# Optimization experiments

Measured on AMD Instinct MI355X. Metric: run time of the kernel, lower is better.

## Reference

```python
import jax, jax.numpy as jnp
import numpy as np

START = 1
NUM_CLASSES = 64  # labels drawn from [0, 64)
EPS = 1e-12       # matches F.normalize eps


def _compactness_loss(embeddings, labels):
    # L2-normalize each embedding (F.normalize, dim=-1)
    norms = jnp.maximum(jnp.linalg.norm(embeddings, axis=-1, keepdims=True), EPS)
    emb = embeddings / norms  # [N, D]

    ones = jnp.ones((emb.shape[0],), dtype=emb.dtype)
    counts = jax.ops.segment_sum(ones, labels, num_segments=NUM_CLASSES)      # [C]
    sums = jax.ops.segment_sum(emb, labels, num_segments=NUM_CLASSES)         # [C, D]

    # per-class mean, then L2-normalize the center (F.normalize, dim=1)
    centers = sums / jnp.maximum(counts, 1.0)[:, None]
    c_norms = jnp.maximum(jnp.linalg.norm(centers, axis=-1, keepdims=True), EPS)
    centers = centers / c_norms  # [C, D]

    # cosine similarity of each sample to its own class center
    sim = jnp.sum(emb * centers[labels], axis=-1)  # [N]

    # per-class mean of (1 - sim), only classes with count > 1 contribute
    per_class_sum = jax.ops.segment_sum(1.0 - sim, labels, num_segments=NUM_CLASSES)  # [C]
    valid = counts > 1.0
    class_loss = jnp.where(valid, per_class_sum / jnp.maximum(counts, 1.0), 0.0)
    n_valid = jnp.sum(valid.astype(emb.dtype))
    return jnp.where(n_valid > 0, jnp.sum(class_loss) / jnp.maximum(n_valid, 1.0), 0.0)


def setup_inputs() -> dict:
    key = jax.random.key(0)
    k1, k2 = jax.random.split(key)
    N, D = 262144, 256
    embeddings = jax.random.normal(k1, (N, D), dtype=jnp.float32)
    labels = jax.random.randint(k2, (N,), 0, NUM_CLASSES, dtype=jnp.int64)
    return {"embeddings": embeddings, "labels": labels, "epoch": 5}


def reference(embeddings, labels, epoch):
    if epoch < START:  # epoch is a static python int
        return jnp.asarray(0.0, dtype=embeddings.dtype)
    return _compactness_loss(embeddings, labels)
```

## Files before the change

### kernel.cpp

```cpp
#include <hip/hip_runtime.h>

#define CLS   64
#define DIM   256
#define PARTS 8
#define HB    256
#define HT    256

typedef float f32x4 __attribute__((ext_vector_type(4)));

__device__ __forceinline__ float wave_sum64(float f) {
    int t;
    t = __builtin_amdgcn_update_dpp(0, __float_as_int(f), 0x111, 0xf, 0xf, false); f += __int_as_float(t);
    t = __builtin_amdgcn_update_dpp(0, __float_as_int(f), 0x112, 0xf, 0xf, false); f += __int_as_float(t);
    t = __builtin_amdgcn_update_dpp(0, __float_as_int(f), 0x114, 0xf, 0xe, false); f += __int_as_float(t);
    t = __builtin_amdgcn_update_dpp(0, __float_as_int(f), 0x118, 0xf, 0xc, false); f += __int_as_float(t);
    t = __builtin_amdgcn_update_dpp(0, __float_as_int(f), 0x142, 0xa, 0xf, false); f += __int_as_float(t);
    t = __builtin_amdgcn_update_dpp(0, __float_as_int(f), 0x143, 0xc, 0xf, false); f += __int_as_float(t);
    return __int_as_float(__builtin_amdgcn_readlane(__float_as_int(f), 63));
}

__global__ __launch_bounds__(HT) void k_hist(const int* __restrict__ labels, int N,
                                             int* __restrict__ hist)
{
    __shared__ int h[CLS];
    if (threadIdx.x < CLS) h[threadIdx.x] = 0;
    __syncthreads();
    const int chunk = (N + gridDim.x - 1) / gridDim.x;
    const int s = blockIdx.x * chunk;
    const int e = min(N, s + chunk);
    for (int i = s + threadIdx.x; i < e; i += blockDim.x)
        atomicAdd(&h[labels[i]], 1);
    __syncthreads();
    if (threadIdx.x < CLS) hist[blockIdx.x * CLS + threadIdx.x] = h[threadIdx.x];
}

__global__ __launch_bounds__(HT) void k_scatter2(
    const int* __restrict__ labels, int N,
    const int* __restrict__ hist,
    int* __restrict__ cstart,
    int* __restrict__ bucket)
{
    __shared__ int t4[4][CLS], p4[4][CLS];
    __shared__ int tot[CLS], pre[CLS], cur[CLS];
    const int tid = threadIdx.x;
    const int c = tid & 63, q = tid >> 6;
    int t = 0, p = 0;
    const int myb = blockIdx.x;
    #pragma unroll 4
    for (int b = q * (HB / 4); b < (q + 1) * (HB / 4); ++b) {
        const int v = hist[b * CLS + c];
        t += v;
        if (b < myb) p += v;
    }
    t4[q][c] = t; p4[q][c] = p;
    __syncthreads();
    if (tid < CLS) {
        tot[tid] = t4[0][tid] + t4[1][tid] + t4[2][tid] + t4[3][tid];
        pre[tid] = p4[0][tid] + p4[1][tid] + p4[2][tid] + p4[3][tid];
    }
    __syncthreads();
    if (tid == 0) {
        int acc = 0;
        for (int j = 0; j < CLS; ++j) { cur[j] = acc + pre[j]; acc += tot[j]; }
    }
    __syncthreads();
    if (myb == 0) {
        if (tid < CLS) cstart[tid] = cur[tid] - pre[tid];
        if (tid == CLS) cstart[CLS] = N;
    }
    const int chunk = (N + gridDim.x - 1) / gridDim.x;
    const int s = myb * chunk;
    const int e = min(N, s + chunk);
    for (int i = s + tid; i < e; i += HT) {
        const int cc = labels[i];
        const int slot = atomicAdd(&cur[cc], 1);
        bucket[slot] = i;
    }
}

__global__ __launch_bounds__(1024) void k_classsum(
    const float* __restrict__ emb, const int* __restrict__ bucket,
    const int* __restrict__ cstart, float* __restrict__ partials)
{
    __shared__ float red[16 * 260];
    const int c    = blockIdx.x >> 3;
    const int part = blockIdx.x & (PARTS - 1);
    const int s0 = cstart[c], s1 = cstart[c + 1];
    const int ccnt = s1 - s0;
    const int p0 = s0 + (int)(((long long)ccnt * part) >> 3);
    const int p1 = s0 + (int)(((long long)ccnt * (part + 1)) >> 3);
    const int wid = threadIdx.x >> 6, lane = threadIdx.x & 63;

    f32x4 acc = {0.f, 0.f, 0.f, 0.f};
    for (int j = p0 + wid; j < p1; j += 16) {
        const int row = bucket[j];
        const f32x4 v = *(reinterpret_cast<const f32x4*>(emb + (size_t)row * DIM) + lane);
        const float ss = wave_sum64(v.x * v.x + v.y * v.y + v.z * v.z + v.w * v.w);
        const float inv = 1.0f / fmaxf(sqrtf(ss), 1e-12f);
        acc.x += v.x * inv; acc.y += v.y * inv; acc.z += v.z * inv; acc.w += v.w * inv;
    }
    float* my = &red[wid * 260 + 4 * lane];
    my[0] = acc.x; my[1] = acc.y; my[2] = acc.z; my[3] = acc.w;
    __syncthreads();
    if (threadIdx.x < DIM) {
        float s = 0.f;
        #pragma unroll
        for (int w = 0; w < 16; ++w) s += red[w * 260 + threadIdx.x];
        partials[(size_t)blockIdx.x * DIM + threadIdx.x] = s;
    }
}

__global__ __launch_bounds__(256) void k_classloss(
    const float* __restrict__ partials, const int* __restrict__ cstart,
    float* __restrict__ closs, float* __restrict__ cvalid)
{
    const int c = blockIdx.x;
    const int d = threadIdx.x;
    float s = 0.f;
    #pragma unroll
    for (int p = 0; p < PARTS; ++p)
        s += partials[(size_t)(c * PARTS + p) * DIM + d];
    const float w = wave_sum64(s * s);
    __shared__ float red[4];
    if ((d & 63) == 0) red[d >> 6] = w;
    __syncthreads();
    if (d == 0) {
        float s2   = red[0] + red[1] + red[2] + red[3];
        float cnt  = (float)(cstart[c + 1] - cstart[c]);
        float invc = 1.0f / fmaxf(cnt, 1.0f);
        float cn   = sqrtf(s2) * invc;
        float dot  = s2 * invc / fmaxf(cn, 1e-12f);
        float pcs  = cnt - dot;
        bool valid = cnt > 1.0f;
        closs[c]  = valid ? pcs * invc : 0.0f;
        cvalid[c] = valid ? 1.0f : 0.0f;
    }
}

__global__ void k_final(const float* __restrict__ closs, const float* __restrict__ cvalid,
                        const int* __restrict__ epoch, float* __restrict__ out)
{
    const int t = threadIdx.x;
    const float sl = wave_sum64(closs[t]);
    const float nv = wave_sum64(cvalid[t]);
    if (t == 0) {
        float res = (nv > 0.0f) ? (sl / fmaxf(nv, 1.0f)) : 0.0f;
        if (epoch[0] < 1) res = 0.0f;
        out[0] = res;
    }
}

extern "C" void kernel_launch(void* const* d_in, const int* in_sizes, int n_in,
                              void* d_out, int out_size, void* d_ws, size_t ws_size,
                              hipStream_t stream)
{
    const float* emb    = (const float*)d_in[0];
    const int*   labels = (const int*)d_in[1];
    const int*   epoch  = (const int*)d_in[2];
    float*       out    = (float*)d_out;
    const int N = in_sizes[0] / DIM;

    char* ws = (char*)d_ws;
    size_t off = 0;
    auto carve = [&](size_t bytes) { size_t o = off; off = (off + bytes + 255) & ~(size_t)255; return o; };
    int*   hist     = (int*)  (ws + carve((size_t)HB * CLS * sizeof(int)));
    int*   cstart   = (int*)  (ws + carve((size_t)(CLS + 1) * sizeof(int)));
    int*   bucket   = (int*)  (ws + carve((size_t)N * sizeof(int)));
    float* partials = (float*)(ws + carve((size_t)CLS * PARTS * DIM * sizeof(float)));
    float* closs    = (float*)(ws + carve((size_t)CLS * sizeof(float)));
    float* cvalid   = (float*)(ws + carve((size_t)CLS * sizeof(float)));
    (void)ws_size;

    k_hist     <<<HB,          HT,   0, stream>>>(labels, N, hist);
    k_scatter2 <<<HB,          HT,   0, stream>>>(labels, N, hist, cstart, bucket);
    k_classsum <<<CLS * PARTS, 1024, 0, stream>>>(emb, bucket, cstart, partials);
    k_classloss<<<CLS,         256,  0, stream>>>(partials, cstart, closs, cvalid);
    k_final    <<<1,           64,   0, stream>>>(closs, cvalid, epoch, out);
}
```

Baseline: 61.78 us.

## Replace global bucket sort with per-block windowed class routing and partial sums

```diff
diff --git a/kernel.cpp b/kernel.cpp
--- a/kernel.cpp
+++ b/kernel.cpp
@@ -1,10 +1,12 @@
 #include <hip/hip_runtime.h>
 
-#define CLS   64
-#define DIM   256
-#define PARTS 8
-#define HB    256
-#define HT    256
+#define CLS 64
+#define DIM 256
+#define NB  256
+#define WIN 1024
+#define WPB 16
+#define CPW 4
+#define P2  4
 
 typedef float f32x4 __attribute__((ext_vector_type(4)));
 
@@ -19,114 +21,106 @@
     return __int_as_float(__builtin_amdgcn_readlane(__float_as_int(f), 63));
 }
 
-__global__ __launch_bounds__(HT) void k_hist(const int* __restrict__ labels, int N,
-                                             int* __restrict__ hist)
+__global__ __launch_bounds__(1024) void k_main(
+    const float* __restrict__ emb, const int* __restrict__ labels, int N,
+    float* __restrict__ partials,
+    float* __restrict__ cnts)
 {
-    __shared__ int h[CLS];
-    if (threadIdx.x < CLS) h[threadIdx.x] = 0;
-    __syncthreads();
-    const int chunk = (N + gridDim.x - 1) / gridDim.x;
-    const int s = blockIdx.x * chunk;
-    const int e = min(N, s + chunk);
-    for (int i = s + threadIdx.x; i < e; i += blockDim.x)
-        atomicAdd(&h[labels[i]], 1);
-    __syncthreads();
-    if (threadIdx.x < CLS) hist[blockIdx.x * CLS + threadIdx.x] = h[threadIdx.x];
-}
+    __shared__ unsigned short lst[WPB][WIN];
+    __shared__ unsigned char  labk[WIN];
+    __shared__ int lcnt[WPB];
 
-__global__ __launch_bounds__(HT) void k_scatter2(
-    const int* __restrict__ labels, int N,
-    const int* __restrict__ hist,
-    int* __restrict__ cstart,
-    int* __restrict__ bucket)
-{
-    __shared__ int t4[4][CLS], p4[4][CLS];
-    __shared__ int tot[CLS], pre[CLS], cur[CLS];
-    const int tid = threadIdx.x;
-    const int c = tid & 63, q = tid >> 6;
-    int t = 0, p = 0;
-    const int myb = blockIdx.x;
-    #pragma unroll 4
-    for (int b = q * (HB / 4); b < (q + 1) * (HB / 4); ++b) {
-        const int v = hist[b * CLS + c];
-        t += v;
-        if (b < myb) p += v;
+    const int tid  = threadIdx.x;
+    const int w    = tid >> 6;
+    const int lane = tid & 63;
+
+    f32x4 a0 = {0,0,0,0}, a1 = {0,0,0,0}, a2 = {0,0,0,0}, a3 = {0,0,0,0};
+    float c0 = 0.f, c1 = 0.f, c2 = 0.f, c3 = 0.f;
+
+    for (int wb = blockIdx.x; (long long)wb * WIN < (long long)N; wb += NB) {
+        const int base  = wb * WIN;
+        const int nrows = min(WIN, N - base);
+        __syncthreads();
+        if (tid < WPB) lcnt[tid] = 0;
+        __syncthreads();
+        if (tid < nrows) {
+            const int c = labels[base + tid];
+            labk[tid] = (unsigned char)(c & (CPW - 1));
+            const int p = atomicAdd(&lcnt[c >> 2], 1);
+            lst[c >> 2][p] = (unsigned short)tid;
+        }
+        __syncthreads();
+
+        const int n = lcnt[w];
+        int   r = (n > 0) ? (int)lst[w][0] : 0;
+        f32x4 v = {0,0,0,0};
+        if (n > 0) v = *(reinterpret_cast<const f32x4*>(emb + (size_t)(base + r) * DIM) + lane);
+        for (int j = 0; j < n; ++j) {
+            const bool more = (j + 1 < n);
+            const int  rn = more ? (int)lst[w][j + 1] : 0;
+            f32x4 vn = {0,0,0,0};
+            if (more) vn = *(reinterpret_cast<const f32x4*>(emb + (size_t)(base + rn) * DIM) + lane);
+            const float ss  = wave_sum64(v.x*v.x + v.y*v.y + v.z*v.z + v.w*v.w);
+            const float inv = 1.0f / fmaxf(sqrtf(ss), 1e-12f);
+            const int   k   = labk[r];
+            const float tx = v.x*inv, ty = v.y*inv, tz = v.z*inv, tw = v.w*inv;
+            if      (k == 0) { a0.x += tx; a0.y += ty; a0.z += tz; a0.w += tw; c0 += 1.f; }
+            else if (k == 1) { a1.x += tx; a1.y += ty; a1.z += tz; a1.w += tw; c1 += 1.f; }
+            else if (k == 2) { a2.x += tx; a2.y += ty; a2.z += tz; a2.w += tw; c2 += 1.f; }
+            else             { a3.x += tx; a3.y += ty; a3.z += tz; a3.w += tw; c3 += 1.f; }
+            r = rn; v = vn;
+        }
     }
-    t4[q][c] = t; p4[q][c] = p;
-    __syncthreads();
-    if (tid < CLS) {
-        tot[tid] = t4[0][tid] + t4[1][tid] + t4[2][tid] + t4[3][tid];
-        pre[tid] = p4[0][tid] + p4[1][tid] + p4[2][tid] + p4[3][tid];
-    }
-    __syncthreads();
-    if (tid == 0) {
-        int acc = 0;
-        for (int j = 0; j < CLS; ++j) { cur[j] = acc + pre[j]; acc += tot[j]; }
-    }
-    __syncthreads();
-    if (myb == 0) {
-        if (tid < CLS) cstart[tid] = cur[tid] - pre[tid];
-        if (tid == CLS) cstart[CLS] = N;
-    }
-    const int chunk = (N + gridDim.x - 1) / gridDim.x;
-    const int s = myb * chunk;
-    const int e = min(N, s + chunk);
-    for (int i = s + tid; i < e; i += HT) {
-        const int cc = labels[i];
-        const int slot = atomicAdd(&cur[cc], 1);
-        bucket[slot] = i;
+
+    const int b = blockIdx.x;
+    {
+        float* p = partials + ((size_t)(w * CPW + 0) * NB + b) * DIM + 4 * lane;
+        *reinterpret_cast<f32x4*>(p) = a0;
+        p = partials + ((size_t)(w * CPW + 1) * NB + b) * DIM + 4 * lane;
+        *reinterpret_cast<f32x4*>(p) = a1;
+        p = partials + ((size_t)(w * CPW + 2) * NB + b) * DIM + 4 * lane;
+        *reinterpret_cast<f32x4*>(p) = a2;
+        p = partials + ((size_t)(w * CPW + 3) * NB + b) * DIM + 4 * lane;
+        *reinterpret_cast<f32x4*>(p) = a3;
+        if (lane == 0) {
+            cnts[(size_t)(w * CPW + 0) * NB + b] = c0;
+            cnts[(size_t)(w * CPW + 1) * NB + b] = c1;
+            cnts[(size_t)(w * CPW + 2) * NB + b] = c2;
+            cnts[(size_t)(w * CPW + 3) * NB + b] = c3;
+        }
     }
 }
 
-__global__ __launch_bounds__(1024) void k_classsum(
-    const float* __restrict__ emb, const int* __restrict__ bucket,
-    const int* __restrict__ cstart, float* __restrict__ partials)
+__global__ __launch_bounds__(256) void k_reduce1(
+    const float* __restrict__ partials, float* __restrict__ red1)
 {
-    __shared__ float red[16 * 260];
-    const int c    = blockIdx.x >> 3;
-    const int part = blockIdx.x & (PARTS - 1);
-    const int s0 = cstart[c], s1 = cstart[c + 1];
-    const int ccnt = s1 - s0;
-    const int p0 = s0 + (int)(((long long)ccnt * part) >> 3);
-    const int p1 = s0 + (int)(((long long)ccnt * (part + 1)) >> 3);
-    const int wid = threadIdx.x >> 6, lane = threadIdx.x & 63;
-
-    f32x4 acc = {0.f, 0.f, 0.f, 0.f};
-    for (int j = p0 + wid; j < p1; j += 16) {
-        const int row = bucket[j];
-        const f32x4 v = *(reinterpret_cast<const f32x4*>(emb + (size_t)row * DIM) + lane);
-        const float ss = wave_sum64(v.x * v.x + v.y * v.y + v.z * v.z + v.w * v.w);
-        const float inv = 1.0f / fmaxf(sqrtf(ss), 1e-12f);
-        acc.x += v.x * inv; acc.y += v.y * inv; acc.z += v.z * inv; acc.w += v.w * inv;
-    }
-    float* my = &red[wid * 260 + 4 * lane];
-    my[0] = acc.x; my[1] = acc.y; my[2] = acc.z; my[3] = acc.w;
-    __syncthreads();
-    if (threadIdx.x < DIM) {
-        float s = 0.f;
-        #pragma unroll
-        for (int w = 0; w < 16; ++w) s += red[w * 260 + threadIdx.x];
-        partials[(size_t)blockIdx.x * DIM + threadIdx.x] = s;
-    }
+    const int c = blockIdx.x >> 2;
+    const int p = blockIdx.x & (P2 - 1);
+    const int d = threadIdx.x;
+    const float* src = partials + ((size_t)c * NB + p * (NB / P2)) * DIM + d;
+    float s = 0.f;
+    #pragma unroll 8
+    for (int b = 0; b < NB / P2; ++b) s += src[(size_t)b * DIM];
+    red1[((size_t)c * P2 + p) * DIM + d] = s;
 }
 
 __global__ __launch_bounds__(256) void k_classloss(
-    const float* __restrict__ partials, const int* __restrict__ cstart,
+    const float* __restrict__ red1, const float* __restrict__ cnts,
     float* __restrict__ closs, float* __restrict__ cvalid)
 {
     const int c = blockIdx.x;
     const int d = threadIdx.x;
     float s = 0.f;
     #pragma unroll
-    for (int p = 0; p < PARTS; ++p)
-        s += partials[(size_t)(c * PARTS + p) * DIM + d];
-    const float w = wave_sum64(s * s);
-    __shared__ float red[4];
-    if ((d & 63) == 0) red[d >> 6] = w;
+    for (int p = 0; p < P2; ++p) s += red1[((size_t)c * P2 + p) * DIM + d];
+    const float w2 = wave_sum64(s * s);
+    const float cw = wave_sum64(cnts[(size_t)c * NB + d]);
+    __shared__ float reds[4], redc[4];
+    if ((d & 63) == 0) { reds[d >> 6] = w2; redc[d >> 6] = cw; }
     __syncthreads();
     if (d == 0) {
-        float s2   = red[0] + red[1] + red[2] + red[3];
-        float cnt  = (float)(cstart[c + 1] - cstart[c]);
+        float s2   = reds[0] + reds[1] + reds[2] + reds[3];
+        float cnt  = redc[0] + redc[1] + redc[2] + redc[3];
         float invc = 1.0f / fmaxf(cnt, 1.0f);
         float cn   = sqrtf(s2) * invc;
         float dot  = s2 * invc / fmaxf(cn, 1e-12f);
@@ -163,17 +157,15 @@
     char* ws = (char*)d_ws;
     size_t off = 0;
     auto carve = [&](size_t bytes) { size_t o = off; off = (off + bytes + 255) & ~(size_t)255; return o; };
-    int*   hist     = (int*)  (ws + carve((size_t)HB * CLS * sizeof(int)));
-    int*   cstart   = (int*)  (ws + carve((size_t)(CLS + 1) * sizeof(int)));
-    int*   bucket   = (int*)  (ws + carve((size_t)N * sizeof(int)));
-    float* partials = (float*)(ws + carve((size_t)CLS * PARTS * DIM * sizeof(float)));
+    float* partials = (float*)(ws + carve((size_t)CLS * NB * DIM * sizeof(float)));
+    float* cnts     = (float*)(ws + carve((size_t)CLS * NB * sizeof(float)));
+    float* red1     = (float*)(ws + carve((size_t)CLS * P2 * DIM * sizeof(float)));
     float* closs    = (float*)(ws + carve((size_t)CLS * sizeof(float)));
     float* cvalid   = (float*)(ws + carve((size_t)CLS * sizeof(float)));
     (void)ws_size;
 
-    k_hist     <<<HB,          HT,   0, stream>>>(labels, N, hist);
-    k_scatter2 <<<HB,          HT,   0, stream>>>(labels, N, hist, cstart, bucket);
-    k_classsum <<<CLS * PARTS, 1024, 0, stream>>>(emb, bucket, cstart, partials);
-    k_classloss<<<CLS,         256,  0, stream>>>(partials, cstart, closs, cvalid);
-    k_final    <<<1,           64,   0, stream>>>(closs, cvalid, epoch, out);
+    k_main     <<<NB,       1024, 0, stream>>>(emb, labels, N, partials, cnts);
+    k_reduce1  <<<CLS * P2, 256,  0, stream>>>(partials, red1);
+    k_classloss<<<CLS,      256,  0, stream>>>(red1, cnts, closs, cvalid);
+    k_final    <<<1,        64,   0, stream>>>(closs, cvalid, epoch, out);
 }
```

Result: slower. 81.41 us (+31.8%).
